# Kernel optimization log

Hardware: AMD Instinct MI355X
Metric: run time of the kernel (lower is better)

The kernel has to match this reference:

```python
import jax, jax.numpy as jnp
import numpy as np

N = 1024
E = 16384
F_IN = 128
H = 64
ALPHA = 0.7


def _gcn(x, src, dst, W, b):
    # PyG GCNConv: add self-loops, symmetric deg^{-1/2} normalization, aggregate at dst.
    loop = jnp.arange(N)
    s = jnp.concatenate([src, loop])
    d = jnp.concatenate([dst, loop])
    deg = jax.ops.segment_sum(jnp.ones_like(s, jnp.float32), d, num_segments=N)
    dinv = jnp.where(deg > 0, jax.lax.rsqrt(deg), 0.0)
    norm = dinv[s] * dinv[d]  # [E+N]
    h = x @ W  # [N,H]
    out = jax.ops.segment_sum(norm[:, None] * h[s], d, num_segments=N)
    return out + b


def _gat(x, src, dst, ew, W, a_src, a_dst, w_edge, a_edge, b):
    # PyG GATConv (heads=1) with scalar edge_attr via lin_edge(edge_dim=1).
    h = x @ W  # [N,H]
    al_s = h @ a_src  # [N]
    al_d = h @ a_dst  # [N]
    loop = jnp.arange(N)
    s = jnp.concatenate([src, loop])
    d = jnp.concatenate([dst, loop])
    ew_l = jnp.concatenate([ew, jnp.full((N,), jnp.mean(ew))])  # fill_value='mean' for self-loops
    c = jnp.dot(w_edge, a_edge)  # scalar: (lin_edge(ew) * att_edge).sum() = ew * c
    e = jax.nn.leaky_relu(al_s[s] + al_d[d] + ew_l * c, 0.2)  # [E+N]
    # segment softmax over destination nodes (every node has a self-loop -> no empty segments)
    emax = jax.ops.segment_max(e, d, num_segments=N)
    ex = jnp.exp(e - emax[d])
    denom = jax.ops.segment_sum(ex, d, num_segments=N)
    alpha = ex / denom[d]
    out = jax.ops.segment_sum(alpha[:, None] * h[s], d, num_segments=N)
    return out + b


def setup_inputs() -> dict:
    key = jax.random.key(0)
    ks = jax.random.split(key, 24)
    g = lambda k, shape, fan: jax.random.normal(k, shape, jnp.float32) / np.sqrt(fan)
    inp = {
        "x": jax.random.normal(ks[0], (N, F_IN), jnp.float32),
        "edge_index_above": jax.random.randint(ks[1], (2, E), 0, N),
        "edge_index_distance": jax.random.randint(ks[2], (2, E), 0, N),
        "edge_weights_distance": jax.random.uniform(ks[3], (E,), jnp.float32),
        # GCNConv1 / GATConv1 (in 128 -> 64)
        "W_gcn1": g(ks[4], (F_IN, H), F_IN), "b_gcn1": jnp.zeros((H,), jnp.float32),
        "W_gat1": g(ks[5], (F_IN, H), F_IN), "att_src1": g(ks[6], (H,), H),
        "att_dst1": g(ks[7], (H,), H), "w_edge1": g(ks[8], (H,), 1),
        "att_edge1": g(ks[9], (H,), H), "b_gat1": jnp.zeros((H,), jnp.float32),
        # GCNConv2 / GATConv2 (64 -> 64)
        "W_gcn2": g(ks[10], (H, H), H), "b_gcn2": jnp.zeros((H,), jnp.float32),
        "W_gat2": g(ks[11], (H, H), H), "att_src2": g(ks[12], (H,), H),
        "att_dst2": g(ks[13], (H,), H), "w_edge2": g(ks[14], (H,), 1),
        "att_edge2": g(ks[15], (H,), H), "b_gat2": jnp.zeros((H,), jnp.float32),
        # GCNConv3 (64 -> 64)
        "W_gcn3": g(ks[16], (H, H), H), "b_gcn3": jnp.zeros((H,), jnp.float32),
        # predictor MLP: Linear(128,64) -> ReLU -> Linear(64,1) -> Sigmoid
        "Wp1": g(ks[17], (2 * H, H), 2 * H), "bp1": jnp.zeros((H,), jnp.float32),
        "Wp2": g(ks[18], (H, 1), H), "bp2": jnp.zeros((1,), jnp.float32),
    }
    return inp


def reference(x, edge_index_above, edge_index_distance, edge_weights_distance,
              W_gcn1, b_gcn1, W_gat1, att_src1, att_dst1, w_edge1, att_edge1, b_gat1,
              W_gcn2, b_gcn2, W_gat2, att_src2, att_dst2, w_edge2, att_edge2, b_gat2,
              W_gcn3, b_gcn3, Wp1, bp1, Wp2, bp2):
    sa, da = edge_index_above[0], edge_index_above[1]
    sd, dd = edge_index_distance[0], edge_index_distance[1]
    ew = edge_weights_distance

    xa1 = jax.nn.relu(_gcn(x, sa, da, W_gcn1, b_gcn1))
    xd1 = jax.nn.relu(_gat(x, sd, dd, ew, W_gat1, att_src1, att_dst1, w_edge1, att_edge1, b_gat1))
    xa2 = jax.nn.relu(_gcn(xa1, sa, da, W_gcn2, b_gcn2))
    xd2 = jax.nn.relu(_gat(xd1, sd, dd, ew, W_gat2, att_src2, att_dst2, w_edge2, att_edge2, b_gat2))
    xc = ALPHA * xa2 + (1.0 - ALPHA) * xd2
    h = jax.nn.relu(_gcn(xc, sa, da, W_gcn3, b_gcn3))  # [N,H]

    # All-pairs predictor, fused: concat([h_i, h_j]) @ Wp1 = h_i @ Wp1[:H] + h_j @ Wp1[H:]
    h1 = h @ Wp1[:H]  # [N,H] contribution of start node
    h2 = h @ Wp1[H:]  # [N,H] contribution of end node
    pre = jax.nn.relu(h1[:, None, :] + h2[None, :, :] + bp1)  # [N,N,H]
    logits = jnp.einsum('ijh,h->ij', pre, Wp2[:, 0]) + bp2[0]  # [N,N]
    return jax.nn.sigmoid(logits).reshape(-1)  # [N*N], row-major = cartesian_prod order
```

## Files before the change

kernel.cpp:

```cpp
#include <hip/hip_runtime.h>

constexpr int NV  = 1024;
constexpr int EV  = 16384;
constexpr int FIN = 128;
constexpr int HD  = 64;
constexpr int CAP = 64;

__device__ __forceinline__ float relu_(float v){ return fmaxf(v, 0.f); }

__device__ __forceinline__ float wsum64(float v){
    for (int off = 32; off; off >>= 1) v += __shfl_xor(v, off, 64);
    return v;
}

__device__ __forceinline__ float sigmoid_(float v){
    return __builtin_amdgcn_rcpf(1.f + __expf(-v));
}

struct KArgs {
    const float* x;
    const int *sa, *da, *sd, *dd;
    const float* ew;
    const float *Wg1, *bg1;
    const float *Wt1, *as1, *ad1, *we1, *ae1, *bt1;
    const float *Wg2, *bg2;
    const float *Wt2, *as2, *ad2, *we2, *ae2, *bt2;
    const float *Wg3, *bg3;
    const float *Wp1, *bp1, *Wp2, *bp2;
    int *cnt_a, *cnt_d;
    float* scal;
    float *al_s1, *al_d1, *al_s2, *al_d2;
    int *ell_a, *ell_d;
    float* ellw_d;
    float *hg1, *hga1, *hg2, *hga2, *hg3, *h1, *h2;
    float* out;
};

__device__ __forceinline__ float gcn_row_w(const KArgs& A, const float* __restrict__ h,
                                           const float* __restrict__ bias, int d, int k)
{
    int deg = min(A.cnt_a[d], CAP);
    int   s_l = A.ell_a[d*CAP + k];
    s_l = (k < deg) ? s_l : 0;
    float c_l = (k < deg) ? rsqrtf((float)A.cnt_a[s_l] + 1.f) : 0.f;
    float dv  = rsqrtf((float)deg + 1.f);
    float a0 = dv * h[d*HD + k], a1=0.f, a2=0.f, a3=0.f,
          a4 = 0.f, a5=0.f, a6=0.f, a7=0.f;
    int degR = (deg + 7) & ~7;
    for (int p = 0; p < degR; p += 8) {
        int   s0 = __shfl(s_l, p,   64), s1 = __shfl(s_l, p+1, 64),
              s2 = __shfl(s_l, p+2, 64), s3 = __shfl(s_l, p+3, 64),
              s4 = __shfl(s_l, p+4, 64), s5 = __shfl(s_l, p+5, 64),
              s6 = __shfl(s_l, p+6, 64), s7 = __shfl(s_l, p+7, 64);
        float c0 = __shfl(c_l, p,   64), c1 = __shfl(c_l, p+1, 64),
              c2 = __shfl(c_l, p+2, 64), c3 = __shfl(c_l, p+3, 64),
              c4 = __shfl(c_l, p+4, 64), c5 = __shfl(c_l, p+5, 64),
              c6 = __shfl(c_l, p+6, 64), c7 = __shfl(c_l, p+7, 64);
        a0 = fmaf(c0, h[s0*HD + k], a0);
        a1 = fmaf(c1, h[s1*HD + k], a1);
        a2 = fmaf(c2, h[s2*HD + k], a2);
        a3 = fmaf(c3, h[s3*HD + k], a3);
        a4 = fmaf(c4, h[s4*HD + k], a4);
        a5 = fmaf(c5, h[s5*HD + k], a5);
        a6 = fmaf(c6, h[s6*HD + k], a6);
        a7 = fmaf(c7, h[s7*HD + k], a7);
    }
    float s = ((a0+a1) + (a2+a3)) + ((a4+a5) + (a6+a7));
    return relu_(fmaf(dv, s, bias[k]));
}

__device__ __forceinline__ float gat_row_w(const KArgs& A, const float* __restrict__ h,
                                           const float* __restrict__ bias,
                                           const float* __restrict__ al_s,
                                           const float* __restrict__ al_d,
                                           float c, float ewm, int d, int k)
{
    int deg = min(A.cnt_d[d], CAP);
    float aD = al_d[d];
    int   s_l = A.ell_d[d*CAP + k];
    float w_l = A.ellw_d[d*CAP + k];
    s_l = (k < deg) ? s_l : 0;
    float e_l = al_s[s_l] + aD + w_l*c;
    e_l = (e_l > 0.f) ? e_l : 0.2f*e_l;
    float x_l = (k < deg) ? __expf(e_l) : 0.f;
    float es  = al_s[d] + aD + ewm*c;
    es = __expf((es > 0.f) ? es : 0.2f*es);
    float den = es + wsum64(x_l);
    float n0 = es * h[d*HD + k], n1=0.f, n2=0.f, n3=0.f,
          n4 = 0.f, n5=0.f, n6=0.f, n7=0.f;
    int degR = (deg + 7) & ~7;
    for (int p = 0; p < degR; p += 8) {
        int   s0 = __shfl(s_l, p,   64), s1 = __shfl(s_l, p+1, 64),
              s2 = __shfl(s_l, p+2, 64), s3 = __shfl(s_l, p+3, 64),
              s4 = __shfl(s_l, p+4, 64), s5 = __shfl(s_l, p+5, 64),
              s6 = __shfl(s_l, p+6, 64), s7 = __shfl(s_l, p+7, 64);
        float x0 = __shfl(x_l, p,   64), x1 = __shfl(x_l, p+1, 64),
              x2 = __shfl(x_l, p+2, 64), x3 = __shfl(x_l, p+3, 64),
              x4 = __shfl(x_l, p+4, 64), x5 = __shfl(x_l, p+5, 64),
              x6 = __shfl(x_l, p+6, 64), x7 = __shfl(x_l, p+7, 64);
        n0 = fmaf(x0, h[s0*HD + k], n0);
        n1 = fmaf(x1, h[s1*HD + k], n1);
        n2 = fmaf(x2, h[s2*HD + k], n2);
        n3 = fmaf(x3, h[s3*HD + k], n3);
        n4 = fmaf(x4, h[s4*HD + k], n4);
        n5 = fmaf(x5, h[s5*HD + k], n5);
        n6 = fmaf(x6, h[s6*HD + k], n6);
        n7 = fmaf(x7, h[s7*HD + k], n7);
    }
    float num = ((n0+n1) + (n2+n3)) + ((n4+n5) + (n6+n7));
    return relu_(fmaf(num, __builtin_amdgcn_rcpf(den), bias[k]));
}

__device__ __forceinline__ float mm_row_lds(const float4* __restrict__ rowF4,
                                            const float* __restrict__ Wf, int j)
{
    float acc = 0.f;
    #pragma unroll
    for (int k4 = 0; k4 < 16; k4++) {
        float4 r = rowF4[k4];
        acc = fmaf(r.x, Wf[(4*k4+0)*64 + j], acc);
        acc = fmaf(r.y, Wf[(4*k4+1)*64 + j], acc);
        acc = fmaf(r.z, Wf[(4*k4+2)*64 + j], acc);
        acc = fmaf(r.w, Wf[(4*k4+3)*64 + j], acc);
    }
    return acc;
}

__global__ __launch_bounds__(256) void k1(KArgs A)
{
    __shared__ __align__(16) float4 Ws[FIN*16];
    const int b = blockIdx.x, tid = threadIdx.x;
    if (b < 512) {
        bool gcn = (b < 256);
        const float4* Wsrc = (const float4*)(gcn ? A.Wg1 : A.Wt1);
        for (int r = tid; r < FIN*16; r += 256) Ws[r] = Wsrc[r];
        __syncthreads();
        int t = (gcn ? b : b-256)*256 + tid, i = t >> 6, j = t & 63;
        const float4* xr = (const float4*)(A.x + i*FIN);
        const float*  Wf = (const float*)Ws;
        float acc = 0.f;
        #pragma unroll
        for (int k4 = 0; k4 < FIN/4; k4++) {
            float4 xv = xr[k4];
            acc = fmaf(xv.x, Wf[(4*k4+0)*64 + j], acc);
            acc = fmaf(xv.y, Wf[(4*k4+1)*64 + j], acc);
            acc = fmaf(xv.z, Wf[(4*k4+2)*64 + j], acc);
            acc = fmaf(xv.w, Wf[(4*k4+3)*64 + j], acc);
        }
        if (gcn) {
            A.hg1[t] = acc;
        } else {
            A.hga1[t] = acc;
            float ps = acc * A.as1[j];
            float pd = acc * A.ad1[j];
            for (int off = 32; off; off >>= 1) {
                ps += __shfl_down(ps, off, 64);
                pd += __shfl_down(pd, off, 64);
            }
            if (j == 0) { A.al_s1[i] = ps; A.al_d1[i] = pd; }
        }
    } else if (b < 576) {
        int e = (b-512)*256 + tid;
        int dA = A.da[e], dD = A.dd[e];
        int pa = atomicAdd(&A.cnt_a[dA], 1);
        if (pa < CAP) A.ell_a[dA*CAP + pa] = A.sa[e];
        float w = A.ew[e];
        int pd = atomicAdd(&A.cnt_d[dD], 1);
        if (pd < CAP) { A.ell_d[dD*CAP + pd] = A.sd[e]; A.ellw_d[dD*CAP + pd] = w; }
        for (int off = 32; off; off >>= 1) w += __shfl_down(w, off, 64);
        if ((tid & 63) == 0) atomicAdd(&A.scal[3], w);
    } else {
        if (tid < 64) {
            float p1 = A.we1[tid]*A.ae1[tid];
            float p2 = A.we2[tid]*A.ae2[tid];
            for (int off = 32; off; off >>= 1) {
                p1 += __shfl_down(p1, off, 64);
                p2 += __shfl_down(p2, off, 64);
            }
            if (tid == 0) { A.scal[1] = p1; A.scal[2] = p2; }
        }
    }
}

__global__ __launch_bounds__(256) void k2(KArgs A)
{
    __shared__ __align__(16) float4 Ws[HD*16];
    __shared__ float rowb[4*64];
    const int b = blockIdx.x, tid = threadIdx.x;
    const float4* Wsrc = (const float4*)((b < 256) ? A.Wg2 : A.Wt2);
    for (int r = tid; r < HD*16; r += 256) Ws[r] = Wsrc[r];
    __syncthreads();
    int w = tid >> 6, k = tid & 63;
    const float* Wf = (const float*)Ws;
    if (b < 256) {
        int d = b*4 + w;
        rowb[w*64 + k] = gcn_row_w(A, A.hg1, A.bg1, d, k);
        A.hg2[d*HD + k] = mm_row_lds((const float4*)(rowb + w*64), Wf, k);
    } else {
        int i = (b-256)*4 + w;
        float c = A.scal[1], ewm = A.scal[3] * (1.f/EV);
        rowb[w*64 + k] = gat_row_w(A, A.hga1, A.bt1, A.al_s1, A.al_d1,
                                   c, ewm, i, k);
        float acc = mm_row_lds((const float4*)(rowb + w*64), Wf, k);
        A.hga2[i*HD + k] = acc;
        float ps = acc * A.as2[k];
        float pd = acc * A.ad2[k];
        for (int off = 32; off; off >>= 1) {
            ps += __shfl_down(ps, off, 64);
            pd += __shfl_down(pd, off, 64);
        }
        if (k == 0) { A.al_s2[i] = ps; A.al_d2[i] = pd; }
    }
}

__global__ __launch_bounds__(256) void k3(KArgs A)
{
    __shared__ __align__(16) float4 Ws[HD*16];
    __shared__ float rows[4*64];
    const int b = blockIdx.x, tid = threadIdx.x;
    for (int r = tid; r < HD*16; r += 256) Ws[r] = ((const float4*)A.Wg3)[r];
    int w = tid >> 6, k = tid & 63;
    int node = b*2 + (w >> 1);
    float v;
    if ((w & 1) == 0) {
        v = 0.7f * gcn_row_w(A, A.hg2, A.bg2, node, k);
    } else {
        float c = A.scal[2], ewm = A.scal[3] * (1.f/EV);
        v = 0.3f * gat_row_w(A, A.hga2, A.bt2, A.al_s2, A.al_d2,
                             c, ewm, node, k);
    }
    rows[w*64 + k] = v;
    __syncthreads();
    if ((w & 1) == 0) {
        const float* Wf = (const float*)Ws;
        const float4* r0 = (const float4*)(rows + w*64);
        const float4* r1 = (const float4*)(rows + (w+1)*64);
        float acc = 0.f;
        #pragma unroll
        for (int k4 = 0; k4 < 16; k4++) {
            float4 ra = r0[k4], rb = r1[k4];
            acc = fmaf(ra.x+rb.x, Wf[(4*k4+0)*64 + k], acc);
            acc = fmaf(ra.y+rb.y, Wf[(4*k4+1)*64 + k], acc);
            acc = fmaf(ra.z+rb.z, Wf[(4*k4+2)*64 + k], acc);
            acc = fmaf(ra.w+rb.w, Wf[(4*k4+3)*64 + k], acc);
        }
        A.hg3[node*HD + k] = acc;
    }
}

__global__ __launch_bounds__(256) void k4(KArgs A)
{
    __shared__ __align__(16) float4 Wp[FIN*16];
    __shared__ float rowb[4*64];
    const int b = blockIdx.x, tid = threadIdx.x;
    for (int r = tid; r < FIN*16; r += 256) Wp[r] = ((const float4*)A.Wp1)[r];
    __syncthreads();
    int w = tid >> 6, k = tid & 63;
    int d = b*4 + w;
    rowb[w*64 + k] = gcn_row_w(A, A.hg3, A.bg3, d, k);
    const float*  Wf = (const float*)Wp;
    const float4* rF = (const float4*)(rowb + w*64);
    float a1 = 0.f, a2 = 0.f;
    #pragma unroll
    for (int k4i = 0; k4i < 16; k4i++) {
        float4 r = rF[k4i];
        a1 = fmaf(r.x, Wf[(4*k4i+0)*64 + k], a1);
        a2 = fmaf(r.x, Wf[(64+4*k4i+0)*64 + k], a2);
        a1 = fmaf(r.y, Wf[(4*k4i+1)*64 + k], a1);
        a2 = fmaf(r.y, Wf[(64+4*k4i+1)*64 + k], a2);
        a1 = fmaf(r.z, Wf[(4*k4i+2)*64 + k], a1);
        a2 = fmaf(r.z, Wf[(64+4*k4i+2)*64 + k], a2);
        a1 = fmaf(r.w, Wf[(4*k4i+3)*64 + k], a1);
        a2 = fmaf(r.w, Wf[(64+4*k4i+3)*64 + k], a2);
    }
    A.h1[d*HD + k] = a1 + A.bp1[k];
    A.h2[d*HD + k] = a2;
}

__global__ __launch_bounds__(256) void k5(KArgs A)
{
    __shared__ float4 s1[32*17], s2[32*17], w2s[16];
    const int tid = threadIdx.x;
    int by = blockIdx.x >> 5, bx = blockIdx.x & 31;
    int i0 = by*32, j0 = bx*32;
    for (int r = tid; r < 512; r += 256) {
        int row = r >> 4, c = r & 15;
        s1[row*17 + c] = ((const float4*)A.h1)[(i0+row)*16 + c];
        s2[row*17 + c] = ((const float4*)A.h2)[(j0+row)*16 + c];
    }
    if (tid < 16) w2s[tid] = ((const float4*)A.Wp2)[tid];
    __syncthreads();
    int ty = tid >> 4, tx = tid & 15;
    float a00=0.f, a01=0.f, a10=0.f, a11=0.f;
    #pragma unroll
    for (int k4 = 0; k4 < 16; k4++) {
        float4 va0 = s1[ty*17 + k4],      va1 = s1[(ty+16)*17 + k4];
        float4 vb0 = s2[tx*17 + k4],      vb1 = s2[(tx+16)*17 + k4];
        float4 wv  = w2s[k4];
#define STEP(c) \
        a00 = fmaf(fmaxf(va0.c+vb0.c, 0.f), wv.c, a00); \
        a01 = fmaf(fmaxf(va0.c+vb1.c, 0.f), wv.c, a01); \
        a10 = fmaf(fmaxf(va1.c+vb0.c, 0.f), wv.c, a10); \
        a11 = fmaf(fmaxf(va1.c+vb1.c, 0.f), wv.c, a11);
        STEP(x) STEP(y) STEP(z) STEP(w)
#undef STEP
    }
    float bb = A.bp2[0];
    int i = i0 + ty, jj = j0 + tx;
    A.out[i*NV + jj]            = sigmoid_(a00+bb);
    A.out[i*NV + jj + 16]       = sigmoid_(a01+bb);
    A.out[(i+16)*NV + jj]       = sigmoid_(a10+bb);
    A.out[(i+16)*NV + jj + 16]  = sigmoid_(a11+bb);
}

extern "C" void kernel_launch(void* const* d_in, const int* in_sizes, int n_in,
                              void* d_out, int out_size, void* d_ws, size_t ws_size,
                              hipStream_t stream)
{
    KArgs A;
    A.x   = (const float*)d_in[0];
    const int* ei_a = (const int*)d_in[1];
    const int* ei_d = (const int*)d_in[2];
    A.ew  = (const float*)d_in[3];
    A.Wg1 = (const float*)d_in[4];  A.bg1 = (const float*)d_in[5];
    A.Wt1 = (const float*)d_in[6];  A.as1 = (const float*)d_in[7];
    A.ad1 = (const float*)d_in[8];  A.we1 = (const float*)d_in[9];
    A.ae1 = (const float*)d_in[10]; A.bt1 = (const float*)d_in[11];
    A.Wg2 = (const float*)d_in[12]; A.bg2 = (const float*)d_in[13];
    A.Wt2 = (const float*)d_in[14]; A.as2 = (const float*)d_in[15];
    A.ad2 = (const float*)d_in[16]; A.we2 = (const float*)d_in[17];
    A.ae2 = (const float*)d_in[18]; A.bt2 = (const float*)d_in[19];
    A.Wg3 = (const float*)d_in[20]; A.bg3 = (const float*)d_in[21];
    A.Wp1 = (const float*)d_in[22]; A.bp1 = (const float*)d_in[23];
    A.Wp2 = (const float*)d_in[24]; A.bp2 = (const float*)d_in[25];
    A.sa = ei_a;      A.da = ei_a + EV;
    A.sd = ei_d;      A.dd = ei_d + EV;
    A.out = (float*)d_out;

    float* W = (float*)d_ws;
    A.cnt_a  = (int*)(W + 0);
    A.cnt_d  = (int*)(W + 1024);
    A.scal   = W + 2048;
    A.al_s1  = W + 2064;
    A.al_d1  = W + 3088;
    A.al_s2  = W + 4112;
    A.al_d2  = W + 5136;
    A.ell_a  = (int*)(W + 6160);
    A.ell_d  = (int*)(W + 71696);
    A.ellw_d = W + 137232;
    A.hg1    = W + 202768;
    A.hga1   = W + 268304;
    A.hg2    = W + 333840;
    A.hga2   = W + 399376;
    A.hg3    = W + 464912;
    A.h1     = W + 530448;
    A.h2     = W + 595984;

    hipMemsetAsync(d_ws, 0, 2064*sizeof(float), stream);

    k1<<<577,  256, 0, stream>>>(A);
    k2<<<512,  256, 0, stream>>>(A);
    k3<<<512,  256, 0, stream>>>(A);
    k4<<<256,  256, 0, stream>>>(A);
    k5<<<1024, 256, 0, stream>>>(A);
}
```

Before: 142.5 us.

## Build ELL adjacency deterministically without atomics and drop workspace memset

Replaces the atomic-based ELL construction with per-node scans: each block stages all destination indices in LDS, and each wavefront counts and prefix-sums matches for its nodes, then writes the neighbours in edge order. This removes the hipMemsetAsync launch and the atomic contention, and makes neighbour order deterministic. The first matmul is also retiled so each block handles 16 nodes with x staged in LDS, and the edge-weight mean is computed by one block instead of with atomics. The trade-off is that every block scans all 16K edges for its 8 nodes, which adds LDS read work, and the 64KB of LDS per block lowers occupancy.

Result: slower. 175.2 us (+23.0%).

```diff
diff --git a/kernel.cpp b/kernel.cpp
--- a/kernel.cpp
+++ b/kernel.cpp
@@ -128,55 +128,94 @@
 
 __global__ __launch_bounds__(256) void k1(KArgs A)
 {
-    __shared__ __align__(16) float4 Ws[FIN*16];
+    __shared__ __align__(16) unsigned char smem[65536];
     const int b = blockIdx.x, tid = threadIdx.x;
-    if (b < 512) {
-        bool gcn = (b < 256);
+    const int w = tid >> 6, lane = tid & 63;
+
+    if (b < 128) {
+        bool gcn = (b < 64);
+        int nb = (gcn ? b : b-64) * 16;
+        float4* WsF = (float4*)smem;
+        float4* xsF = (float4*)(smem + 32768);
         const float4* Wsrc = (const float4*)(gcn ? A.Wg1 : A.Wt1);
-        for (int r = tid; r < FIN*16; r += 256) Ws[r] = Wsrc[r];
+        for (int r = tid; r < FIN*16; r += 256) WsF[r] = Wsrc[r];
+        const float4* xsrc = (const float4*)(A.x + nb*FIN);
+        for (int r = tid; r < 16*FIN/4; r += 256) xsF[r] = xsrc[r];
         __syncthreads();
-        int t = (gcn ? b : b-256)*256 + tid, i = t >> 6, j = t & 63;
-        const float4* xr = (const float4*)(A.x + i*FIN);
-        const float*  Wf = (const float*)Ws;
-        float acc = 0.f;
-        #pragma unroll
-        for (int k4 = 0; k4 < FIN/4; k4++) {
-            float4 xv = xr[k4];
-            acc = fmaf(xv.x, Wf[(4*k4+0)*64 + j], acc);
-            acc = fmaf(xv.y, Wf[(4*k4+1)*64 + j], acc);
-            acc = fmaf(xv.z, Wf[(4*k4+2)*64 + j], acc);
-            acc = fmaf(xv.w, Wf[(4*k4+3)*64 + j], acc);
+        const float* Wf = (const float*)smem;
+        const float* xs = (const float*)(smem + 32768);
+        float asv = 0.f, adv = 0.f;
+        if (!gcn) { asv = A.as1[lane]; adv = A.ad1[lane]; }
+        for (int nt = 0; nt < 4; nt++) {
+            int lr = w*4 + nt;
+            int node = nb + lr;
+            const float4* xrF = (const float4*)(xs + lr*FIN);
+            float acc = 0.f;
+            #pragma unroll
+            for (int f4 = 0; f4 < FIN/4; f4++) {
+                float4 xv = xrF[f4];
+                acc = fmaf(xv.x, Wf[(4*f4+0)*64 + lane], acc);
+                acc = fmaf(xv.y, Wf[(4*f4+1)*64 + lane], acc);
+                acc = fmaf(xv.z, Wf[(4*f4+2)*64 + lane], acc);
+                acc = fmaf(xv.w, Wf[(4*f4+3)*64 + lane], acc);
+            }
+            if (gcn) {
+                A.hg1[node*HD + lane] = acc;
+            } else {
+                A.hga1[node*HD + lane] = acc;
+                float ps = wsum64(acc * asv);
+                float pd = wsum64(acc * adv);
+                if (lane == 0) { A.al_s1[node] = ps; A.al_d1[node] = pd; }
+            }
         }
-        if (gcn) {
-            A.hg1[t] = acc;
-        } else {
-            A.hga1[t] = acc;
-            float ps = acc * A.as1[j];
-            float pd = acc * A.ad1[j];
-            for (int off = 32; off; off >>= 1) {
-                ps += __shfl_down(ps, off, 64);
-                pd += __shfl_down(pd, off, 64);
+    } else if (b < 384) {
+        bool ga = (b < 256);
+        int blk = ga ? (b-128) : (b-256);
+        const int* dsts = ga ? A.da : A.dd;
+        const int* srcs = ga ? A.sa : A.sd;
+        int* ell = ga ? A.ell_a : A.ell_d;
+        int* cnt = ga ? A.cnt_a : A.cnt_d;
+        int4* dstS4 = (int4*)smem;
+        const int4* dsrc4 = (const int4*)dsts;
+        for (int r = tid; r < EV/4; r += 256) dstS4[r] = dsrc4[r];
+        __syncthreads();
+        const int* dstS = (const int*)smem;
+        for (int nt = 0; nt < 2; nt++) {
+            int node = blk*8 + w*2 + nt;
+            int cntl = 0;
+            for (int it = 0; it < EV/64; it++)
+                cntl += (dstS[it*64 + lane] == node) ? 1 : 0;
+            int inc = cntl;
+            #pragma unroll
+            for (int off = 1; off < 64; off <<= 1) {
+                int t = __shfl_up(inc, off, 64);
+                if (lane >= off) inc += t;
             }
-            if (j == 0) { A.al_s1[i] = ps; A.al_d1[i] = pd; }
+            int pos = inc - cntl;
+            int deg = __shfl(inc, 63, 64);
+            for (int it = 0; it < EV/64; it++) {
+                int e = it*64 + lane;
+                if (dstS[e] == node) {
+                    if (pos < CAP) {
+                        ell[node*CAP + pos] = srcs[e];
+                        if (!ga) A.ellw_d[node*CAP + pos] = A.ew[e];
+                    }
+                    pos++;
+                }
+            }
+            if (lane == 0) cnt[node] = deg;
         }
-    } else if (b < 576) {
-        int e = (b-512)*256 + tid;
-        int dA = A.da[e], dD = A.dd[e];
-        int pa = atomicAdd(&A.cnt_a[dA], 1);
-        if (pa < CAP) A.ell_a[dA*CAP + pa] = A.sa[e];
-        float w = A.ew[e];
-        int pd = atomicAdd(&A.cnt_d[dD], 1);
-        if (pd < CAP) { A.ell_d[dD*CAP + pd] = A.sd[e]; A.ellw_d[dD*CAP + pd] = w; }
-        for (int off = 32; off; off >>= 1) w += __shfl_down(w, off, 64);
-        if ((tid & 63) == 0) atomicAdd(&A.scal[3], w);
     } else {
+        float* red = (float*)smem;
+        float s = 0.f;
+        for (int i = tid; i < EV; i += 256) s += A.ew[i];
+        s = wsum64(s);
+        if (lane == 0) red[w] = s;
+        __syncthreads();
+        if (tid == 0) A.scal[3] = (red[0]+red[1]) + (red[2]+red[3]);
         if (tid < 64) {
-            float p1 = A.we1[tid]*A.ae1[tid];
-            float p2 = A.we2[tid]*A.ae2[tid];
-            for (int off = 32; off; off >>= 1) {
-                p1 += __shfl_down(p1, off, 64);
-                p2 += __shfl_down(p2, off, 64);
-            }
+            float p1 = wsum64(A.we1[tid]*A.ae1[tid]);
+            float p2 = wsum64(A.we2[tid]*A.ae2[tid]);
             if (tid == 0) { A.scal[1] = p1; A.scal[2] = p2; }
         }
     }
@@ -356,9 +395,7 @@
     A.h1     = W + 530448;
     A.h2     = W + 595984;
 
-    hipMemsetAsync(d_ws, 0, 2064*sizeof(float), stream);
-
-    k1<<<577,  256, 0, stream>>>(A);
+    k1<<<385,  256, 0, stream>>>(A);
     k2<<<512,  256, 0, stream>>>(A);
     k3<<<512,  256, 0, stream>>>(A);
     k4<<<256,  256, 0, stream>>>(A);
```
